# Kernel optimization log

Measured on AMD Instinct MI355X. Metric: run time of the kernel, lower is better.

## Reference

```python
import jax, jax.numpy as jnp
import numpy as np

VOCAB = 32000
HIDDEN = 2048
NLAYERS = 6
BATCH = 512


def setup_inputs() -> dict:
    key = jax.random.key(0)
    k1, k2, k3, k4 = jax.random.split(key, 4)
    state = jax.random.normal(k1, (BATCH, HIDDEN), dtype=jnp.float32)
    token = jax.random.randint(k2, (BATCH,), 0, VOCAB, dtype=jnp.int32)
    ih = jax.random.normal(k3, (NLAYERS, VOCAB, HIDDEN), dtype=jnp.float32) * 0.02
    hh = jax.random.normal(k4, (NLAYERS, HIDDEN, HIDDEN), dtype=jnp.float32) * 0.02
    return {"state": state, "token": token, "ih": ih, "hh": hh}


def reference(state, token, ih, hh):
    # Per layer: state = tanh(state + (state @ hh[i]) * ih[i][token])
    n_layers = ih.shape[0]
    for i in range(n_layers):
        gate = ih[i][token]                  # [B, H] embedding gather
        state = jnp.tanh(state + jnp.matmul(state, hh[i]) * gate)
    return state
```

## Files before the change

kernel.cpp:

```cpp
#include <hip/hip_runtime.h>
#include <hip/hip_bf16.h>
#include <cstdint>
#include <cstddef>

#define VOCAB 32000
#define HIDDEN 2048
#define NLAYERS 6
#define BATCH 512

#define BM 64
#define BN 64
#define BK 64
#define SPLITK 4
#define KC (HIDDEN / SPLITK)
#define NT (KC / BK)

typedef __attribute__((ext_vector_type(8))) short bf16x8;
typedef __attribute__((ext_vector_type(4))) float f32x4;

__device__ __forceinline__ unsigned short f2bf(float f) {
  unsigned u = __builtin_bit_cast(unsigned, f);
  u += 0x7fffu + ((u >> 16) & 1u);
  return (unsigned short)(u >> 16);
}

__device__ __forceinline__ float bf2f(unsigned short h) {
  return __builtin_bit_cast(float, (unsigned)h << 16);
}

__device__ __forceinline__ float tanh_fast(float x) {
  x = fminf(15.f, fmaxf(-15.f, x));
  float e = __expf(2.f * x);
  return (e - 1.f) / (e + 1.f);
}

__device__ __forceinline__ void gload_lds16(const void* g, void* l) {
  __builtin_amdgcn_global_load_lds(
      (const __attribute__((address_space(1))) void*)g,
      (__attribute__((address_space(3))) void*)l, 16, 0, 0);
}

__global__ __launch_bounds__(256) void k_prep(const float* __restrict__ hh,
                                              unsigned short* __restrict__ bt,
                                              const float* __restrict__ state,
                                              unsigned short* __restrict__ stb) {
  const int l = blockIdx.z;
  const int t = threadIdx.x;
  if (l == NLAYERS) {
    const int bid = blockIdx.y * 32 + blockIdx.x;
    const int i = (bid * 256 + t) * 4;
    float4 v = *(const float4*)(state + i);
    union { unsigned short h[4]; uint2 u; } o;
    o.h[0] = f2bf(v.x); o.h[1] = f2bf(v.y); o.h[2] = f2bf(v.z); o.h[3] = f2bf(v.w);
    *(uint2*)(stb + i) = o.u;
    return;
  }
  __shared__ unsigned short tile[64][72];
  const int n0 = blockIdx.x * 64;
  const int k0 = blockIdx.y * 64;
  const float* src = hh + ((size_t)l * HIDDEN + k0) * HIDDEN + n0;
  const int cr = t >> 4;
  const int cc = (t & 15) * 4;
#pragma unroll
  for (int p = 0; p < 4; ++p) {
    const int r = p * 16 + cr;
    float4 v = *(const float4*)(src + (size_t)r * HIDDEN + cc);
    tile[r][cc + 0] = f2bf(v.x);
    tile[r][cc + 1] = f2bf(v.y);
    tile[r][cc + 2] = f2bf(v.z);
    tile[r][cc + 3] = f2bf(v.w);
  }
  __syncthreads();
  const int nl = t >> 2;
  const int kk = (t & 3) * 16;
  unsigned short tmp[16] __attribute__((aligned(16)));
#pragma unroll
  for (int j = 0; j < 16; ++j) tmp[j] = tile[kk + j][nl];
  unsigned short* dst = bt + ((size_t)l * HIDDEN + n0 + nl) * HIDDEN + k0 + kk;
  *(uint4*)(dst) = *(const uint4*)(tmp);
  *(uint4*)(dst + 8) = *(const uint4*)(tmp + 8);
}

__global__ __launch_bounds__(256, 4) void k_gemm(const unsigned short* __restrict__ A,
                                                 const unsigned short* __restrict__ Bt,
                                                 unsigned short* __restrict__ part) {
  __shared__ __attribute__((aligned(16))) unsigned short As[2][BM][BK];
  __shared__ __attribute__((aligned(16))) unsigned short Bs[2][BN][BK];

  const int wgid = blockIdx.x;
  const int xcd = wgid & 7;
  const int idx = wgid >> 3;
  const int n0 = (xcd * 4 + (idx & 3)) * BN;
  const int m0 = ((idx >> 2) & 7) * BM;
  const int kz = idx >> 5;
  const int kbase = kz * KC;
  const int t = threadIdx.x;
  const int lane = t & 63;
  const int wid = t >> 6;
  const int wm = (wid >> 1) * 32;
  const int wn = (wid & 1) * 32;

  f32x4 zero = {0.f, 0.f, 0.f, 0.f};
  f32x4 acc[2][2];
  acc[0][0] = zero; acc[0][1] = zero; acc[1][0] = zero; acc[1][1] = zero;

  const int r0 = t >> 3;
  const int sc = ((t & 7) ^ (r0 & 7)) * 8;
  const unsigned short* gA = A + (size_t)(m0 + r0) * HIDDEN + kbase + sc;
  const unsigned short* gB = Bt + (size_t)(n0 + r0) * HIDDEN + kbase + sc;
  char* lA = (char*)&As[0][0][0] + wid * 1024;
  char* lB = (char*)&Bs[0][0][0] + wid * 1024;

#define STAGE(buf, kt)                                                     \
  do {                                                                     \
    const int ko = (kt)*BK;                                                \
    gload_lds16(gA + ko, lA + (buf)*8192);                                 \
    gload_lds16(gA + 32 * HIDDEN + ko, lA + (buf)*8192 + 4096);            \
    gload_lds16(gB + ko, lB + (buf)*8192);                                 \
    gload_lds16(gB + 32 * HIDDEN + ko, lB + (buf)*8192 + 4096);            \
  } while (0)

  const int row_a0 = wm + (lane & 15);
  const int row_a1 = row_a0 + 16;
  const int row_b0 = wn + (lane & 15);
  const int row_b1 = row_b0 + 16;
  const int q = lane >> 4;

#define COMPUTE(buf)                                                                    \
  do {                                                                                  \
    _Pragma("unroll") for (int ks = 0; ks < 2; ++ks) {                                  \
      const int cnk = ks * 4 + q;                                                       \
      bf16x8 a0 = *(const bf16x8*)&As[buf][row_a0][(cnk ^ (row_a0 & 7)) * 8];           \
      bf16x8 a1 = *(const bf16x8*)&As[buf][row_a1][(cnk ^ (row_a1 & 7)) * 8];           \
      bf16x8 b0 = *(const bf16x8*)&Bs[buf][row_b0][(cnk ^ (row_b0 & 7)) * 8];           \
      bf16x8 b1 = *(const bf16x8*)&Bs[buf][row_b1][(cnk ^ (row_b1 & 7)) * 8];           \
      acc[0][0] = __builtin_amdgcn_mfma_f32_16x16x32_bf16(a0, b0, acc[0][0], 0, 0, 0);  \
      acc[0][1] = __builtin_amdgcn_mfma_f32_16x16x32_bf16(a0, b1, acc[0][1], 0, 0, 0);  \
      acc[1][0] = __builtin_amdgcn_mfma_f32_16x16x32_bf16(a1, b0, acc[1][0], 0, 0, 0);  \
      acc[1][1] = __builtin_amdgcn_mfma_f32_16x16x32_bf16(a1, b1, acc[1][1], 0, 0, 0);  \
    }                                                                                   \
  } while (0)

  STAGE(0, 0);
  __syncthreads();
  for (int kt = 0; kt < NT; ++kt) {
    const int buf = kt & 1;
    if (kt + 1 < NT) STAGE(buf ^ 1, kt + 1);
    COMPUTE(buf);
    __syncthreads();
  }

  unsigned short* p = part + (size_t)kz * ((size_t)BATCH * HIDDEN);
  const int rb = m0 + wm + (q << 2);
  const int cb = n0 + wn + (lane & 15);
#pragma unroll
  for (int fm = 0; fm < 2; ++fm)
#pragma unroll
    for (int fn = 0; fn < 2; ++fn)
#pragma unroll
      for (int j = 0; j < 4; ++j)
        p[(size_t)(rb + fm * 16 + j) * HIDDEN + cb + fn * 16] = f2bf(acc[fm][fn][j]);
}

__global__ __launch_bounds__(256) void k_reduce(const unsigned short* __restrict__ part,
                                                const float* __restrict__ prev,
                                                const float* __restrict__ ihl,
                                                const int* __restrict__ token,
                                                float* __restrict__ outf,
                                                unsigned short* __restrict__ outb) {
  const int idx = (blockIdx.x * 256 + threadIdx.x) * 4;
  const int m = idx >> 11;
  const int n = idx & 2047;
  const size_t MN = (size_t)BATCH * HIDDEN;
  float s[4] = {0.f, 0.f, 0.f, 0.f};
#pragma unroll
  for (int kz = 0; kz < SPLITK; ++kz) {
    union { uint2 u; unsigned short h[4]; } v;
    v.u = *(const uint2*)(part + kz * MN + idx);
#pragma unroll
    for (int j = 0; j < 4; ++j) s[j] += bf2f(v.h[j]);
  }
  float4 pv = *(const float4*)(prev + idx);
  const int tok = token[m];
  float4 g = *(const float4*)(ihl + (size_t)tok * HIDDEN + n);
  float4 r;
  r.x = tanh_fast(pv.x + s[0] * g.x);
  r.y = tanh_fast(pv.y + s[1] * g.y);
  r.z = tanh_fast(pv.z + s[2] * g.z);
  r.w = tanh_fast(pv.w + s[3] * g.w);
  *(float4*)(outf + idx) = r;
  if (outb) {
    union { unsigned short h[4]; uint2 u; } o;
    o.h[0] = f2bf(r.x); o.h[1] = f2bf(r.y); o.h[2] = f2bf(r.z); o.h[3] = f2bf(r.w);
    *(uint2*)(outb + idx) = o.u;
  }
}

extern "C" void kernel_launch(void* const* d_in, const int* in_sizes, int n_in,
                              void* d_out, int out_size, void* d_ws, size_t ws_size,
                              hipStream_t stream) {
  const float* state = (const float*)d_in[0];
  const int* token = (const int*)d_in[1];
  const float* ih = (const float*)d_in[2];
  const float* hh = (const float*)d_in[3];
  float* out = (float*)d_out;

  char* ws = (char*)d_ws;
  unsigned short* bt = (unsigned short*)ws;
  size_t off = (size_t)NLAYERS * HIDDEN * HIDDEN * 2;
  unsigned short* stb = (unsigned short*)(ws + off);
  off += (size_t)BATCH * HIDDEN * 2;
  float* sf = (float*)(ws + off);
  off += (size_t)BATCH * HIDDEN * 4;
  unsigned short* part = (unsigned short*)(ws + off);

  k_prep<<<dim3(HIDDEN / 64, HIDDEN / 64, NLAYERS + 1), 256, 0, stream>>>(hh, bt, state, stb);

  for (int l = 0; l < NLAYERS; ++l) {
    const bool last = (l == NLAYERS - 1);
    k_gemm<<<dim3(SPLITK * (HIDDEN / BN) * (BATCH / BM)), 256, 0, stream>>>(
        stb, bt + (size_t)l * HIDDEN * HIDDEN, part);
    k_reduce<<<dim3((BATCH * HIDDEN) / 1024), 256, 0, stream>>>(
        part, l == 0 ? state : sf, ih + (size_t)l * VOCAB * HIDDEN, token,
        last ? out : sf, last ? nullptr : stb);
  }
}
```

Baseline: 126.8 us.

## Overlap next layer's weight transpose with current layer's GEMM launch

The up-front prep kernel used to transpose and convert all six layers' hh weights to bf16. Now it converts only layer 0 plus the state. Each later layer's transpose runs as extra workgroups appended to the previous layer's GEMM grid, sharing one LDS buffer. The aim is to hide the large weight conversion behind the split-K GEMM, which on its own launches only 1024 blocks. The risk is that transpose blocks compete with GEMM blocks for bandwidth and compute units, making the GEMM kernels longer.

```diff
diff --git a/kernel.cpp b/kernel.cpp
--- a/kernel.cpp
+++ b/kernel.cpp
@@ -14,6 +14,9 @@
 #define SPLITK 4
 #define KC (HIDDEN / SPLITK)
 #define NT (KC / BK)
+#define GEMM_BLOCKS (SPLITK * (HIDDEN / BN) * (BATCH / BM))
+#define TRANS_BLOCKS ((HIDDEN / 64) * (HIDDEN / 64))
+#define CVT_BLOCKS ((BATCH * HIDDEN) / 1024)
 
 typedef __attribute__((ext_vector_type(8))) short bf16x8;
 typedef __attribute__((ext_vector_type(4))) float f32x4;
@@ -40,25 +43,11 @@
       (__attribute__((address_space(3))) void*)l, 16, 0, 0);
 }
 
-__global__ __launch_bounds__(256) void k_prep(const float* __restrict__ hh,
-                                              unsigned short* __restrict__ bt,
-                                              const float* __restrict__ state,
-                                              unsigned short* __restrict__ stb) {
-  const int l = blockIdx.z;
-  const int t = threadIdx.x;
-  if (l == NLAYERS) {
-    const int bid = blockIdx.y * 32 + blockIdx.x;
-    const int i = (bid * 256 + t) * 4;
-    float4 v = *(const float4*)(state + i);
-    union { unsigned short h[4]; uint2 u; } o;
-    o.h[0] = f2bf(v.x); o.h[1] = f2bf(v.y); o.h[2] = f2bf(v.z); o.h[3] = f2bf(v.w);
-    *(uint2*)(stb + i) = o.u;
-    return;
-  }
-  __shared__ unsigned short tile[64][72];
-  const int n0 = blockIdx.x * 64;
-  const int k0 = blockIdx.y * 64;
-  const float* src = hh + ((size_t)l * HIDDEN + k0) * HIDDEN + n0;
+__device__ __forceinline__ void transpose_tile(const float* __restrict__ src_layer,
+                                               unsigned short* __restrict__ dst_layer,
+                                               int n0, int k0, int t,
+                                               unsigned short (*tile)[72]) {
+  const float* src = src_layer + (size_t)k0 * HIDDEN + n0;
   const int cr = t >> 4;
   const int cc = (t & 15) * 4;
 #pragma unroll
@@ -76,25 +65,53 @@
   unsigned short tmp[16] __attribute__((aligned(16)));
 #pragma unroll
   for (int j = 0; j < 16; ++j) tmp[j] = tile[kk + j][nl];
-  unsigned short* dst = bt + ((size_t)l * HIDDEN + n0 + nl) * HIDDEN + k0 + kk;
+  unsigned short* dst = dst_layer + (size_t)(n0 + nl) * HIDDEN + k0 + kk;
   *(uint4*)(dst) = *(const uint4*)(tmp);
   *(uint4*)(dst + 8) = *(const uint4*)(tmp + 8);
 }
 
-__global__ __launch_bounds__(256, 4) void k_gemm(const unsigned short* __restrict__ A,
-                                                 const unsigned short* __restrict__ Bt,
-                                                 unsigned short* __restrict__ part) {
-  __shared__ __attribute__((aligned(16))) unsigned short As[2][BM][BK];
-  __shared__ __attribute__((aligned(16))) unsigned short Bs[2][BN][BK];
-
-  const int wgid = blockIdx.x;
-  const int xcd = wgid & 7;
-  const int idx = wgid >> 3;
+__global__ __launch_bounds__(256) void k_prep0(const float* __restrict__ hh0,
+                                               unsigned short* __restrict__ bt0,
+                                               const float* __restrict__ state,
+                                               unsigned short* __restrict__ stb) {
+  __shared__ unsigned short tile[64][72];
+  const int wg = blockIdx.x;
+  const int t = threadIdx.x;
+  if (wg < TRANS_BLOCKS) {
+    transpose_tile(hh0, bt0, (wg & 31) * 64, (wg >> 5) * 64, t, tile);
+    return;
+  }
+  const int i = ((wg - TRANS_BLOCKS) * 256 + t) * 4;
+  float4 v = *(const float4*)(state + i);
+  union { unsigned short h[4]; uint2 u; } o;
+  o.h[0] = f2bf(v.x); o.h[1] = f2bf(v.y); o.h[2] = f2bf(v.z); o.h[3] = f2bf(v.w);
+  *(uint2*)(stb + i) = o.u;
+}
+
+__global__ __launch_bounds__(256, 4) void k_gemm_trans(
+    const unsigned short* __restrict__ A, const unsigned short* __restrict__ Bt,
+    unsigned short* __restrict__ part,
+    const float* __restrict__ hhNext, unsigned short* __restrict__ btNext) {
+  __shared__ __attribute__((aligned(16))) unsigned char smem[32768];
+  const int t = threadIdx.x;
+  const int wg = blockIdx.x;
+
+  if (wg >= GEMM_BLOCKS) {
+    const int tn = wg - GEMM_BLOCKS;
+    transpose_tile(hhNext, btNext, (tn & 31) * 64, (tn >> 5) * 64, t,
+                   (unsigned short(*)[72])smem);
+    return;
+  }
+
+  unsigned short (*As)[BM][BK] = (unsigned short(*)[BM][BK])smem;
+  unsigned short (*Bs)[BN][BK] = (unsigned short(*)[BN][BK])(smem + 16384);
+
+  const int xcd = wg & 7;
+  const int idx = wg >> 3;
   const int n0 = (xcd * 4 + (idx & 3)) * BN;
   const int m0 = ((idx >> 2) & 7) * BM;
   const int kz = idx >> 5;
   const int kbase = kz * KC;
-  const int t = threadIdx.x;
   const int lane = t & 63;
   const int wid = t >> 6;
   const int wm = (wid >> 1) * 32;
@@ -108,16 +125,16 @@
   const int sc = ((t & 7) ^ (r0 & 7)) * 8;
   const unsigned short* gA = A + (size_t)(m0 + r0) * HIDDEN + kbase + sc;
   const unsigned short* gB = Bt + (size_t)(n0 + r0) * HIDDEN + kbase + sc;
-  char* lA = (char*)&As[0][0][0] + wid * 1024;
-  char* lB = (char*)&Bs[0][0][0] + wid * 1024;
-
-#define STAGE(buf, kt)                                                     \
-  do {                                                                     \
-    const int ko = (kt)*BK;                                                \
-    gload_lds16(gA + ko, lA + (buf)*8192);                                 \
-    gload_lds16(gA + 32 * HIDDEN + ko, lA + (buf)*8192 + 4096);            \
-    gload_lds16(gB + ko, lB + (buf)*8192);                                 \
-    gload_lds16(gB + 32 * HIDDEN + ko, lB + (buf)*8192 + 4096);            \
+  char* lA = (char*)smem + wid * 1024;
+  char* lB = (char*)smem + 16384 + wid * 1024;
+
+#define STAGE(buf, kt)                                          \
+  do {                                                          \
+    const int ko = (kt)*BK;                                     \
+    gload_lds16(gA + ko, lA + (buf)*8192);                      \
+    gload_lds16(gA + 32 * HIDDEN + ko, lA + (buf)*8192 + 4096); \
+    gload_lds16(gB + ko, lB + (buf)*8192);                      \
+    gload_lds16(gB + 32 * HIDDEN + ko, lB + (buf)*8192 + 4096); \
   } while (0)
 
   const int row_a0 = wm + (lane & 15);
@@ -214,12 +231,15 @@
   off += (size_t)BATCH * HIDDEN * 4;
   unsigned short* part = (unsigned short*)(ws + off);
 
-  k_prep<<<dim3(HIDDEN / 64, HIDDEN / 64, NLAYERS + 1), 256, 0, stream>>>(hh, bt, state, stb);
+  k_prep0<<<dim3(TRANS_BLOCKS + CVT_BLOCKS), 256, 0, stream>>>(hh, bt, state, stb);
 
   for (int l = 0; l < NLAYERS; ++l) {
     const bool last = (l == NLAYERS - 1);
-    k_gemm<<<dim3(SPLITK * (HIDDEN / BN) * (BATCH / BM)), 256, 0, stream>>>(
-        stb, bt + (size_t)l * HIDDEN * HIDDEN, part);
+    const int nblocks = GEMM_BLOCKS + (last ? 0 : TRANS_BLOCKS);
+    k_gemm_trans<<<dim3(nblocks), 256, 0, stream>>>(
+        stb, bt + (size_t)l * HIDDEN * HIDDEN, part,
+        last ? nullptr : hh + (size_t)(l + 1) * HIDDEN * HIDDEN,
+        last ? nullptr : bt + (size_t)(l + 1) * HIDDEN * HIDDEN);
     k_reduce<<<dim3((BATCH * HIDDEN) / 1024), 256, 0, stream>>>(
         part, l == 0 ? state : sf, ih + (size_t)l * VOCAB * HIDDEN, token,
         last ? out : sf, last ? nullptr : stb);
```

Result: faster. 113.1 us (-10.8%).
